# Optimization experiments

Measured on AMD Instinct MI355X. Metric: run time of the kernel, lower is better.

The kernel has to match this reference:

```python
import jax, jax.numpy as jnp
import numpy as np

S, P, D, KH, KW = 1, 1, 1, 3, 3  # stride, padding, dilation, kernel
EPS = 1e-5


def _conv(x, w, b):
    y = jax.lax.conv_general_dilated(
        x, w, (S, S), [(P, P), (P, P)], rhs_dilation=(D, D),
        dimension_numbers=('NCHW', 'OIHW', 'NCHW'))
    return y + b[None, :, None, None]


def _deform_conv(x, offset, mask, w, b):
    # torchvision deform_conv2d v2 semantics: offset layout [B, 2*K, Ho, Wo]
    # with (dy, dx) interleaved per kernel tap; bilinear sampling w/ zero pad.
    B, C, H, W = x.shape
    K = KH * KW
    Ho, Wo = offset.shape[2], offset.shape[3]
    ki, kj = jnp.meshgrid(jnp.arange(KH), jnp.arange(KW), indexing='ij')
    ki = ki.reshape(K).astype(offset.dtype)
    kj = kj.reshape(K).astype(offset.dtype)
    base_y = (jnp.arange(Ho, dtype=offset.dtype) * S - P)[None, None, :, None] + (ki * D)[None, :, None, None]
    base_x = (jnp.arange(Wo, dtype=offset.dtype) * S - P)[None, None, None, :] + (kj * D)[None, :, None, None]
    off = offset.reshape(B, K, 2, Ho, Wo)
    py = base_y + off[:, :, 0]  # [B,K,Ho,Wo]
    px = base_x + off[:, :, 1]
    y0 = jnp.floor(py)
    x0 = jnp.floor(px)
    ly = py - y0
    lx = px - x0
    y0i = y0.astype(jnp.int32)
    x0i = x0.astype(jnp.int32)

    def corner(iy, ix, wgt):
        valid = (iy >= 0) & (iy < H) & (ix >= 0) & (ix < W)
        iyc = jnp.clip(iy, 0, H - 1)
        ixc = jnp.clip(ix, 0, W - 1)
        # gather -> [B, C, K, Ho, Wo]
        v = jax.vmap(lambda img, a, bb: img[:, a, bb])(x, iyc, ixc)
        return v * (wgt * valid)[:, None]

    val = (corner(y0i, x0i, (1 - ly) * (1 - lx))
           + corner(y0i, x0i + 1, (1 - ly) * lx)
           + corner(y0i + 1, x0i, ly * (1 - lx))
           + corner(y0i + 1, x0i + 1, ly * lx))
    val = val * mask[:, None]  # modulation, mask: [B,K,Ho,Wo]
    O = w.shape[0]
    out = jnp.einsum('bckhw,ock->bohw', val, w.reshape(O, C, K))
    return out + b[None, :, None, None]


def setup_inputs() -> dict:
    key = jax.random.key(0)
    ks = jax.random.split(key, 8)
    B, Cin, H, W = 16, 64, 64, 64
    Cout, K = 128, KH * KW
    fan = Cin * K
    x = jax.random.normal(ks[0], (B, Cin, H, W), jnp.float32)
    w_p = jax.random.normal(ks[1], (2 * K, Cin, KH, KW), jnp.float32) * 0.02
    b_p = jax.random.normal(ks[2], (2 * K,), jnp.float32) * 0.01
    w_m = jax.random.normal(ks[3], (K, Cin, KH, KW), jnp.float32) * 0.02
    b_m = jax.random.normal(ks[4], (K,), jnp.float32) * 0.01
    w_d = jax.random.normal(ks[5], (Cout, Cin, KH, KW), jnp.float32) / np.sqrt(fan)
    b_d = jax.random.normal(ks[6], (Cout,), jnp.float32) * 0.01
    gamma = jnp.ones((Cout,), jnp.float32)
    beta = jnp.zeros((Cout,), jnp.float32)
    return {"x": x, "w_p": w_p, "b_p": b_p, "w_m": w_m, "b_m": b_m,
            "w_d": w_d, "b_d": b_d, "gamma": gamma, "beta": beta}


def reference(x, w_p, b_p, w_m, b_m, w_d, b_d, gamma, beta):
    offset = _conv(x, w_p, b_p)                 # [B, 2K, Ho, Wo]
    mask = jax.nn.sigmoid(_conv(x, w_m, b_m))   # [B, K, Ho, Wo]
    y = _deform_conv(x, offset, mask, w_d, b_d)
    # BatchNorm2d (training-mode batch stats, biased variance, eps=1e-5)
    mu = y.mean(axis=(0, 2, 3), keepdims=True)
    var = y.var(axis=(0, 2, 3), keepdims=True)
    yn = (y - mu) * jax.lax.rsqrt(var + EPS)
    yn = yn * gamma[None, :, None, None] + beta[None, :, None, None]
    return jax.nn.gelu(yn, approximate=False)  # nn.GELU default = exact erf
```

## Files before the change

kernel.cpp:

```cpp
#include <hip/hip_runtime.h>
#include <math.h>

#define BB 16
#define CIN 64
#define HH 64
#define WW 64
#define COUT 128
#define HW 4096
#define CK 576
#define VROW 612

typedef __attribute__((ext_vector_type(8))) short short8;
typedef __attribute__((ext_vector_type(4))) short short4v;
typedef __attribute__((ext_vector_type(4))) float f32x4;

#define WT_OFF    0
#define WPM_OFF   36864
#define XH_OFF    46080
#define YB_OFF    2143232
#define SAB_OFF   6337536
#define STAT_OFF  6337792

__device__ __forceinline__ short f2bf(float f) {
    union { float f; unsigned u; } cv; cv.f = f;
    unsigned u = cv.u;
    unsigned r = (u + 0x7fffu + ((u >> 16) & 1u)) >> 16;
    return (short)r;
}
__device__ __forceinline__ float bf2f(short s) {
    union { unsigned u; float f; } cv;
    cv.u = ((unsigned)(unsigned short)s) << 16;
    return cv.f;
}
__device__ __forceinline__ unsigned cvt_pk_bf16(float lo, float hi) {
    unsigned r;
    asm("v_cvt_pk_bf16_f32 %0, %1, %2" : "=v"(r) : "v"(lo), "v"(hi));
    return r;
}

__global__ __launch_bounds__(256) void k_prep(const float* __restrict__ x,
                                              const float* __restrict__ wd,
                                              const float* __restrict__ wp,
                                              const float* __restrict__ wm,
                                              short* __restrict__ xh,
                                              short* __restrict__ wt2,
                                              short* __restrict__ wpm2) {
    const int blk = blockIdx.x;
    if (blk < 1024) {
        __shared__ float t[64][65];
        const int b    = blk >> 6;
        const int pos0 = (blk & 63) << 6;
        const int a    = threadIdx.x & 63;
        const int q    = threadIdx.x >> 6;
#pragma unroll
        for (int i = 0; i < 16; ++i) {
            int c = i * 4 + q;
            t[c][a] = x[((size_t)(b * CIN + c)) * HW + pos0 + a];
        }
        __syncthreads();
#pragma unroll
        for (int i = 0; i < 16; ++i) {
            int p = i * 4 + q;
            xh[((size_t)b * HW + pos0 + p) * CIN + a] = f2bf(t[a][p]);
        }
        return;
    }
    int i = (blk - 1024) * 256 + threadIdx.x;
    if (i < 18 * 128 * 32) {
        int kc  = i >> 12;
        int rem = i & 4095;
        int co  = rem >> 5;
        int kl  = rem & 31;
        int kk  = kc * 32 + kl;
        int k   = kk >> 6;
        int c   = kk & 63;
        wt2[i] = f2bf(wd[co * CK + c * 9 + k]);
        return;
    }
    i -= 18 * 128 * 32;
    if (i < 18 * 32 * 32) {
        int kc  = i >> 10;
        int rem = i & 1023;
        int t   = rem >> 5;
        int kl  = rem & 31;
        int kk  = kc * 32 + kl;
        int k   = kk >> 6;
        int c   = kk & 63;
        float v = 0.f;
        if (t < 18)      v = wp[t * CK + c * 9 + k];
        else if (t < 27) v = wm[(t - 18) * CK + c * 9 + k];
        wpm2[i] = f2bf(v);
    }
}

__device__ __forceinline__ short8 conv_a(const short* __restrict__ xb,
                                         int ho, int wo, int lk, int kc) {
    const int k  = kc >> 1;
    const int c0 = (kc & 1) * 32 + lk * 8;
    const int yy = ho - 1 + k / 3;
    const int xx = wo - 1 + k % 3;
    const bool valid = ((unsigned)yy < 64u) & ((unsigned)xx < 64u);
    const int yyc = min(max(yy, 0), 63);
    const int xxc = min(max(xx, 0), 63);
    short8 a = *(const short8*)&xb[(((yyc << 6) + xxc) << 6) + c0];
    if (!valid) a = (short8)0;
    return a;
}

#define MPB 32
__global__ __launch_bounds__(512) void k_deform(const short* __restrict__ xh,
                                                const short* __restrict__ wt2,
                                                const short* __restrict__ wpm2,
                                                const float* __restrict__ bp,
                                                const float* __restrict__ bm,
                                                const float* __restrict__ bd,
                                                short* __restrict__ yb,
                                                float* __restrict__ gstat) {
    __shared__ short     val[MPB * VROW];
    __shared__ float     s_pm2[2][32][33];
    __shared__ unsigned  s_yx[MPB * 9];
    __shared__ _Float16  s_wh[MPB * 9 * 4];

    const int bid  = blockIdx.x;
    const int swz  = (bid & 7) * 256 + (bid >> 3);
    const int pos0 = swz * MPB;
    const int b   = pos0 >> 12;
    const int ho  = (pos0 >> 6) & 63;
    const int wo0 = pos0 & 63;
    const int tid = threadIdx.x;
    const int wv   = tid >> 6;
    const int lane = tid & 63;
    const int l15  = lane & 15;
    const int lk   = lane >> 4;

    const short* xb = xh + (size_t)b * HW * CIN;

    {
        const int mw = wv & 1;
        const int nw = (wv >> 1) & 1;
        const int kh = wv >> 2;
        const int t  = nw * 16 + l15;
        const short* wr = wpm2 + t * 32 + lk * 8;
        const int wo = wo0 + mw * 16 + l15;
        f32x4 acc = (f32x4)(0.f);
#pragma unroll
        for (int kc = kh * 9; kc < kh * 9 + 9; ++kc) {
            short8 a  = conv_a(xb, ho, wo, lk, kc);
            short8 bf = *(const short8*)&wr[kc * 1024];
            acc = __builtin_amdgcn_mfma_f32_16x16x32_bf16(a, bf, acc, 0, 0, 0);
        }
#pragma unroll
        for (int j = 0; j < 4; ++j)
            s_pm2[kh][t][mw * 16 + lk * 4 + j] = acc[j];
    }
    __syncthreads();

    if (tid < MPB * 9) {
        int k = tid >> 5;
        int p = tid & 31;
        int wo = wo0 + p;
        float dy = s_pm2[0][2 * k    ][p] + s_pm2[1][2 * k    ][p] + bp[2 * k];
        float dx = s_pm2[0][2 * k + 1][p] + s_pm2[1][2 * k + 1][p] + bp[2 * k + 1];
        float mm = s_pm2[0][18 + k   ][p] + s_pm2[1][18 + k   ][p] + bm[k];
        float m  = 1.f / (1.f + expf(-mm));
        float py = (float)(ho - 1 + k / 3) + dy;
        float px = (float)(wo - 1 + k % 3) + dx;
        float fy = floorf(py), fx = floorf(px);
        float ly = py - fy, lx = px - fx;
        int y0 = (int)fy, x0 = (int)fx;
        int y1 = y0 + 1, x1 = x0 + 1;
        float vy0 = ((unsigned)y0 < 64u) ? 1.f : 0.f;
        float vy1 = ((unsigned)y1 < 64u) ? 1.f : 0.f;
        float vx0 = ((unsigned)x0 < 64u) ? 1.f : 0.f;
        float vx1 = ((unsigned)x1 < 64u) ? 1.f : 0.f;
        int y0c = min(max(y0, 0), 63), y1c = min(max(y1, 0), 63);
        int x0c = min(max(x0, 0), 63), x1c = min(max(x1, 0), 63);
        int tt = p * 9 + k;
        s_yx[tt] = (unsigned)y0c | ((unsigned)y1c << 8) | ((unsigned)x0c << 16) | ((unsigned)x1c << 24);
        s_wh[tt * 4 + 0] = (_Float16)((1.f - ly) * (1.f - lx) * m * vy0 * vx0);
        s_wh[tt * 4 + 1] = (_Float16)((1.f - ly) * lx * m * vy0 * vx1);
        s_wh[tt * 4 + 2] = (_Float16)(ly * (1.f - lx) * m * vy1 * vx0);
        s_wh[tt * 4 + 3] = (_Float16)(ly * lx * m * vy1 * vx1);
    }
    __syncthreads();

    {
        const int g  = tid >> 3;
        const int li = tid & 7;
        const int c0 = li * 8;
#pragma unroll
        for (int it = 0; it < 5; ++it) {
            int pr = it * 64 + g;
            if (pr < MPB * 9) {
                unsigned yx = s_yx[pr];
                int y0 = yx & 255, y1 = (yx >> 8) & 255;
                int x0 = (yx >> 16) & 255, x1 = yx >> 24;
                float w0 = (float)s_wh[pr * 4 + 0], w1 = (float)s_wh[pr * 4 + 1];
                float w2 = (float)s_wh[pr * 4 + 2], w3 = (float)s_wh[pr * 4 + 3];
                short8 v00 = *(const short8*)&xb[(((y0 << 6) + x0) << 6) + c0];
                short8 v01 = *(const short8*)&xb[(((y0 << 6) + x1) << 6) + c0];
                short8 v10 = *(const short8*)&xb[(((y1 << 6) + x0) << 6) + c0];
                short8 v11 = *(const short8*)&xb[(((y1 << 6) + x1) << 6) + c0];
                int p = pr / 9, k = pr - p * 9;
                union { unsigned u[4]; short8 s; } pk;
#pragma unroll
                for (int h = 0; h < 4; ++h) {
                    float fa = w0 * bf2f(v00[2*h])   + w1 * bf2f(v01[2*h])
                             + w2 * bf2f(v10[2*h])   + w3 * bf2f(v11[2*h]);
                    float fb = w0 * bf2f(v00[2*h+1]) + w1 * bf2f(v01[2*h+1])
                             + w2 * bf2f(v10[2*h+1]) + w3 * bf2f(v11[2*h+1]);
                    pk.u[h] = cvt_pk_bf16(fa, fb);
                }
                *(short8*)&val[p * VROW + k * 68 + c0] = pk.s;
            }
        }
    }
    __syncthreads();

    f32x4 acc0 = (f32x4)(0.f);
    f32x4 acc1 = (f32x4)(0.f);
    const short* wq = wt2 + (size_t)(wv * 16 + l15) * 32 + lk * 8;
    const int arow0 = l15 * VROW + lk * 8;
    const int arow1 = (l15 + 16) * VROW + lk * 8;
#pragma unroll
    for (int kc = 0; kc < 18; ++kc) {
        const int koff = (kc >> 1) * 68 + (kc & 1) * 32;
        short8 a0 = *(const short8*)&val[arow0 + koff];
        short8 a1 = *(const short8*)&val[arow1 + koff];
        short8 bf = *(const short8*)&wq[kc * 4096];
        acc0 = __builtin_amdgcn_mfma_f32_16x16x32_bf16(a0, bf, acc0, 0, 0, 0);
        acc1 = __builtin_amdgcn_mfma_f32_16x16x32_bf16(a1, bf, acc1, 0, 0, 0);
    }

    const int co = wv * 16 + l15;
    {
        float bias = bd[co];
        short* ybp = yb + ((size_t)(b * COUT + co)) * HW + ho * WW + wo0;
        union { unsigned u[2]; short4v s; } o0, o1;
        o0.u[0] = cvt_pk_bf16(acc0[0] + bias, acc0[1] + bias);
        o0.u[1] = cvt_pk_bf16(acc0[2] + bias, acc0[3] + bias);
        *(short4v*)&ybp[lk * 4] = o0.s;
        o1.u[0] = cvt_pk_bf16(acc1[0] + bias, acc1[1] + bias);
        o1.u[1] = cvt_pk_bf16(acc1[2] + bias, acc1[3] + bias);
        *(short4v*)&ybp[16 + lk * 4] = o1.s;
    }
    float s0 = acc0[0] + acc0[1] + acc0[2] + acc0[3]
             + acc1[0] + acc1[1] + acc1[2] + acc1[3];
    float q0 = acc0[0]*acc0[0] + acc0[1]*acc0[1] + acc0[2]*acc0[2] + acc0[3]*acc0[3]
             + acc1[0]*acc1[0] + acc1[1]*acc1[1] + acc1[2]*acc1[2] + acc1[3]*acc1[3];
    s0 += __shfl_xor(s0, 16); s0 += __shfl_xor(s0, 32);
    q0 += __shfl_xor(q0, 16); q0 += __shfl_xor(q0, 32);
    if (lane < 16) {
        float* slot = gstat + (bid & 63) * 256;
        atomicAdd(&slot[wv * 16 + lane],       s0);
        atomicAdd(&slot[128 + wv * 16 + lane], q0);
    }
}

__global__ __launch_bounds__(128) void k_finalize(const float* __restrict__ gstat,
                                                  const float* __restrict__ bd,
                                                  const float* __restrict__ gamma,
                                                  const float* __restrict__ beta,
                                                  float* __restrict__ sAB) {
    int c = threadIdx.x;
    float s = 0.f, q = 0.f;
    for (int sl = 0; sl < 64; ++sl) {
        s += gstat[sl * 256 + c];
        q += gstat[sl * 256 + 128 + c];
    }
    const float invN = 1.f / (float)(BB * HW);
    float mean_acc = s * invN;
    float var = q * invN - mean_acc * mean_acc;
    float mean_y = mean_acc + bd[c];
    float A = gamma[c] * rsqrtf(var + 1e-5f);
    sAB[c]       = A;
    sAB[128 + c] = beta[c] - mean_y * A;
}

__global__ __launch_bounds__(256) void k_norm_gelu(const short* __restrict__ yb,
                                                   const float* __restrict__ sAB,
                                                   float* __restrict__ out) {
    int i8 = blockIdx.x * 256 + threadIdx.x;
    if (i8 >= (BB * COUT * HW) / 8) return;
    int c = (i8 >> 9) & 127;
    float A  = sAB[c];
    float Bc = sAB[128 + c];
    short8 v = *(const short8*)&yb[(size_t)i8 * 8];
    float4 r0, r1;
    float t;
    t = bf2f(v[0]) * A + Bc; r0.x = 0.5f * t * (1.f + erff(t * 0.70710678118654752f));
    t = bf2f(v[1]) * A + Bc; r0.y = 0.5f * t * (1.f + erff(t * 0.70710678118654752f));
    t = bf2f(v[2]) * A + Bc; r0.z = 0.5f * t * (1.f + erff(t * 0.70710678118654752f));
    t = bf2f(v[3]) * A + Bc; r0.w = 0.5f * t * (1.f + erff(t * 0.70710678118654752f));
    t = bf2f(v[4]) * A + Bc; r1.x = 0.5f * t * (1.f + erff(t * 0.70710678118654752f));
    t = bf2f(v[5]) * A + Bc; r1.y = 0.5f * t * (1.f + erff(t * 0.70710678118654752f));
    t = bf2f(v[6]) * A + Bc; r1.z = 0.5f * t * (1.f + erff(t * 0.70710678118654752f));
    t = bf2f(v[7]) * A + Bc; r1.w = 0.5f * t * (1.f + erff(t * 0.70710678118654752f));
    *(float4*)&out[(size_t)i8 * 8]     = r0;
    *(float4*)&out[(size_t)i8 * 8 + 4] = r1;
}

extern "C" void kernel_launch(void* const* d_in, const int* in_sizes, int n_in,
                              void* d_out, int out_size, void* d_ws, size_t ws_size,
                              hipStream_t stream) {
    const float* x     = (const float*)d_in[0];
    const float* w_p   = (const float*)d_in[1];
    const float* b_p   = (const float*)d_in[2];
    const float* w_m   = (const float*)d_in[3];
    const float* b_m   = (const float*)d_in[4];
    const float* w_d   = (const float*)d_in[5];
    const float* b_d   = (const float*)d_in[6];
    const float* gamma = (const float*)d_in[7];
    const float* beta  = (const float*)d_in[8];
    float* ws  = (float*)d_ws;
    float* out = (float*)d_out;

    short* wt2  = (short*)(ws + WT_OFF);
    short* wpm2 = (short*)(ws + WPM_OFF);
    short* xh   = (short*)(ws + XH_OFF);
    short* yb   = (short*)(ws + YB_OFF);
    float* sAB  = ws + SAB_OFF;
    float* gstat= ws + STAT_OFF;

    hipMemsetAsync(gstat, 0, 64 * 256 * sizeof(float), stream);
    k_prep<<<dim3(1024 + 360), dim3(256), 0, stream>>>(x, w_d, w_p, w_m, xh, wt2, wpm2);
    k_deform<<<dim3(BB * HW / MPB), dim3(512), 0, stream>>>(xh, wt2, wpm2, b_p, b_m, b_d, yb, gstat);
    k_finalize<<<dim3(1), dim3(128), 0, stream>>>(gstat, b_d, gamma, beta, sAB);
    k_norm_gelu<<<dim3(BB * COUT * HW / 8 / 256), dim3(256), 0, stream>>>(yb, sAB, out);
}
```

Measured before the change: 86.45 us.

## Software-pipeline global loads in deform kernel phases with inline asm waitcnt

Replaces the compiler-scheduled loops in the offset conv, the bilinear gather and the main MFMA loop with manually multi-buffered global loads issued through inline asm. Explicit s_waitcnt vmcnt values keep several loads in flight while earlier MFMAs or blends execute. The finalize reduction is split into four independent accumulators. This is meant to hide global memory latency, at the cost of more registers and fragile hand-counted waitcnt values that the compiler cannot check.

After: 84.50 us. -2.3%, faster.

```diff
diff --git a/kernel.cpp b/kernel.cpp
--- a/kernel.cpp
+++ b/kernel.cpp
@@ -93,20 +93,6 @@
     }
 }
 
-__device__ __forceinline__ short8 conv_a(const short* __restrict__ xb,
-                                         int ho, int wo, int lk, int kc) {
-    const int k  = kc >> 1;
-    const int c0 = (kc & 1) * 32 + lk * 8;
-    const int yy = ho - 1 + k / 3;
-    const int xx = wo - 1 + k % 3;
-    const bool valid = ((unsigned)yy < 64u) & ((unsigned)xx < 64u);
-    const int yyc = min(max(yy, 0), 63);
-    const int xxc = min(max(xx, 0), 63);
-    short8 a = *(const short8*)&xb[(((yyc << 6) + xxc) << 6) + c0];
-    if (!valid) a = (short8)0;
-    return a;
-}
-
 #define MPB 32
 __global__ __launch_bounds__(512) void k_deform(const short* __restrict__ xh,
                                                 const short* __restrict__ wt2,
@@ -136,19 +122,49 @@
     const short* xb = xh + (size_t)b * HW * CIN;
 
     {
-        const int mw = wv & 1;
-        const int nw = (wv >> 1) & 1;
-        const int kh = wv >> 2;
-        const int t  = nw * 16 + l15;
+        const int mw  = wv & 1;
+        const int nw  = (wv >> 1) & 1;
+        const int kh  = wv >> 2;
+        const int kc0 = kh * 9;
+        const int t   = nw * 16 + l15;
         const short* wr = wpm2 + t * 32 + lk * 8;
         const int wo = wo0 + mw * 16 + l15;
+
+        short8 ab[3], bb[3];
+        int    va[3];
+
+#define P0_ISSUE(slot, kcl)                                                  \
+        {   int kc = kc0 + (kcl);                                            \
+            int k = kc >> 1; int c0 = (kc & 1) * 32 + lk * 8;                \
+            int yy = ho - 1 + k / 3;                                         \
+            int xx = wo - 1 + k % 3;                                         \
+            va[slot] = (((unsigned)yy < 64u) & ((unsigned)xx < 64u)) ? -1 : 0; \
+            int yyc = min(max(yy, 0), 63), xxc = min(max(xx, 0), 63);        \
+            const short* ap_ = xb + (((yyc << 6) + xxc) << 6) + c0;          \
+            const short* bp_ = wr + kc * 1024;                               \
+            asm volatile("global_load_dwordx4 %0, %1, off"                   \
+                         : "=&v"(ab[slot]) : "v"(ap_));                      \
+            asm volatile("global_load_dwordx4 %0, %1, off"                   \
+                         : "=&v"(bb[slot]) : "v"(bp_));                      \
+        }
+
+#define P0_STEP(i, VM)                                                      \
+        {   asm volatile("s_waitcnt vmcnt(" #VM ")"                          \
+                         : "+v"(ab[(i) % 3]), "+v"(bb[(i) % 3]));            \
+            short8 a = ab[(i) % 3];                                          \
+            if (!va[(i) % 3]) a = (short8)0;                                 \
+            acc = __builtin_amdgcn_mfma_f32_16x16x32_bf16(a, bb[(i) % 3], acc, 0, 0, 0); \
+            if ((i) + 3 < 9) P0_ISSUE((i) % 3, (i) + 3);                     \
+        }
+
         f32x4 acc = (f32x4)(0.f);
-#pragma unroll
-        for (int kc = kh * 9; kc < kh * 9 + 9; ++kc) {
-            short8 a  = conv_a(xb, ho, wo, lk, kc);
-            short8 bf = *(const short8*)&wr[kc * 1024];
-            acc = __builtin_amdgcn_mfma_f32_16x16x32_bf16(a, bf, acc, 0, 0, 0);
-        }
+        P0_ISSUE(0, 0) P0_ISSUE(1, 1) P0_ISSUE(2, 2)
+        P0_STEP(0, 4) P0_STEP(1, 4) P0_STEP(2, 4)
+        P0_STEP(3, 4) P0_STEP(4, 4) P0_STEP(5, 4)
+        P0_STEP(6, 4) P0_STEP(7, 2) P0_STEP(8, 0)
+#undef P0_ISSUE
+#undef P0_STEP
+
 #pragma unroll
         for (int j = 0; j < 4; ++j)
             s_pm2[kh][t][mw * 16 + lk * 4 + j] = acc[j];
@@ -188,31 +204,73 @@
         const int g  = tid >> 3;
         const int li = tid & 7;
         const int c0 = li * 8;
-#pragma unroll
-        for (int it = 0; it < 5; ++it) {
-            int pr = it * 64 + g;
-            if (pr < MPB * 9) {
-                unsigned yx = s_yx[pr];
-                int y0 = yx & 255, y1 = (yx >> 8) & 255;
-                int x0 = (yx >> 16) & 255, x1 = yx >> 24;
-                float w0 = (float)s_wh[pr * 4 + 0], w1 = (float)s_wh[pr * 4 + 1];
-                float w2 = (float)s_wh[pr * 4 + 2], w3 = (float)s_wh[pr * 4 + 3];
-                short8 v00 = *(const short8*)&xb[(((y0 << 6) + x0) << 6) + c0];
-                short8 v01 = *(const short8*)&xb[(((y0 << 6) + x1) << 6) + c0];
-                short8 v10 = *(const short8*)&xb[(((y1 << 6) + x0) << 6) + c0];
-                short8 v11 = *(const short8*)&xb[(((y1 << 6) + x1) << 6) + c0];
-                int p = pr / 9, k = pr - p * 9;
-                union { unsigned u[4]; short8 s; } pk;
-#pragma unroll
-                for (int h = 0; h < 4; ++h) {
-                    float fa = w0 * bf2f(v00[2*h])   + w1 * bf2f(v01[2*h])
-                             + w2 * bf2f(v10[2*h])   + w3 * bf2f(v11[2*h]);
-                    float fb = w0 * bf2f(v00[2*h+1]) + w1 * bf2f(v01[2*h+1])
-                             + w2 * bf2f(v10[2*h+1]) + w3 * bf2f(v11[2*h+1]);
-                    pk.u[h] = cvt_pk_bf16(fa, fb);
-                }
-                *(short8*)&val[p * VROW + k * 68 + c0] = pk.s;
+        short8 cb[2][4];
+
+#define P2_ISSUE(slot, IT)                                                   \
+        {   int pr = (IT) * 64 + g;                                          \
+            unsigned yx = s_yx[pr];                                          \
+            int y0 = yx & 255, y1 = (yx >> 8) & 255;                         \
+            int x0 = (yx >> 16) & 255, x1 = yx >> 24;                        \
+            asm volatile("global_load_dwordx4 %0, %1, off"                   \
+                : "=&v"(cb[slot][0]) : "v"(xb + (((y0 << 6) + x0) << 6) + c0)); \
+            asm volatile("global_load_dwordx4 %0, %1, off"                   \
+                : "=&v"(cb[slot][1]) : "v"(xb + (((y0 << 6) + x1) << 6) + c0)); \
+            asm volatile("global_load_dwordx4 %0, %1, off"                   \
+                : "=&v"(cb[slot][2]) : "v"(xb + (((y1 << 6) + x0) << 6) + c0)); \
+            asm volatile("global_load_dwordx4 %0, %1, off"                   \
+                : "=&v"(cb[slot][3]) : "v"(xb + (((y1 << 6) + x1) << 6) + c0)); \
+        }
+
+#define P2_BLEND(slot, IT, VM)                                               \
+        {   asm volatile("s_waitcnt vmcnt(" #VM ")"                          \
+                : "+v"(cb[slot][0]), "+v"(cb[slot][1]),                      \
+                  "+v"(cb[slot][2]), "+v"(cb[slot][3]));                     \
+            int pr = (IT) * 64 + g;                                          \
+            int p = pr / 9, k = pr - p * 9;                                  \
+            float w0 = (float)s_wh[pr * 4 + 0], w1 = (float)s_wh[pr * 4 + 1];\
+            float w2 = (float)s_wh[pr * 4 + 2], w3 = (float)s_wh[pr * 4 + 3];\
+            union { unsigned u[4]; short8 s; } pk;                           \
+            _Pragma("unroll")                                                \
+            for (int h = 0; h < 4; ++h) {                                    \
+                float fa = w0*bf2f(cb[slot][0][2*h])   + w1*bf2f(cb[slot][1][2*h])   \
+                         + w2*bf2f(cb[slot][2][2*h])   + w3*bf2f(cb[slot][3][2*h]);  \
+                float fb = w0*bf2f(cb[slot][0][2*h+1]) + w1*bf2f(cb[slot][1][2*h+1]) \
+                         + w2*bf2f(cb[slot][2][2*h+1]) + w3*bf2f(cb[slot][3][2*h+1]);\
+                pk.u[h] = cvt_pk_bf16(fa, fb);                               \
+            }                                                                \
+            *(short8*)&val[p * VROW + k * 68 + c0] = pk.s;                   \
+        }
+
+        P2_ISSUE(0, 0)
+        P2_ISSUE(1, 1) P2_BLEND(0, 0, 4)
+        P2_ISSUE(0, 2) P2_BLEND(1, 1, 4)
+        P2_ISSUE(1, 3) P2_BLEND(0, 2, 4)
+        P2_BLEND(1, 3, 0)
+#undef P2_ISSUE
+#undef P2_BLEND
+
+        if (g < 32) {
+            int pr = 256 + g;
+            unsigned yx = s_yx[pr];
+            int y0 = yx & 255, y1 = (yx >> 8) & 255;
+            int x0 = (yx >> 16) & 255, x1 = yx >> 24;
+            float w0 = (float)s_wh[pr * 4 + 0], w1 = (float)s_wh[pr * 4 + 1];
+            float w2 = (float)s_wh[pr * 4 + 2], w3 = (float)s_wh[pr * 4 + 3];
+            short8 v00 = *(const short8*)&xb[(((y0 << 6) + x0) << 6) + c0];
+            short8 v01 = *(const short8*)&xb[(((y0 << 6) + x1) << 6) + c0];
+            short8 v10 = *(const short8*)&xb[(((y1 << 6) + x0) << 6) + c0];
+            short8 v11 = *(const short8*)&xb[(((y1 << 6) + x1) << 6) + c0];
+            int p = pr / 9, k = pr - p * 9;
+            union { unsigned u[4]; short8 s; } pk;
+#pragma unroll
+            for (int h = 0; h < 4; ++h) {
+                float fa = w0 * bf2f(v00[2*h])   + w1 * bf2f(v01[2*h])
+                         + w2 * bf2f(v10[2*h])   + w3 * bf2f(v11[2*h]);
+                float fb = w0 * bf2f(v00[2*h+1]) + w1 * bf2f(v01[2*h+1])
+                         + w2 * bf2f(v10[2*h+1]) + w3 * bf2f(v11[2*h+1]);
+                pk.u[h] = cvt_pk_bf16(fa, fb);
             }
+            *(short8*)&val[p * VROW + k * 68 + c0] = pk.s;
         }
     }
     __syncthreads();
@@ -222,14 +280,31 @@
     const short* wq = wt2 + (size_t)(wv * 16 + l15) * 32 + lk * 8;
     const int arow0 = l15 * VROW + lk * 8;
     const int arow1 = (l15 + 16) * VROW + lk * 8;
-#pragma unroll
-    for (int kc = 0; kc < 18; ++kc) {
-        const int koff = (kc >> 1) * 68 + (kc & 1) * 32;
-        short8 a0 = *(const short8*)&val[arow0 + koff];
-        short8 a1 = *(const short8*)&val[arow1 + koff];
-        short8 bf = *(const short8*)&wq[kc * 4096];
-        acc0 = __builtin_amdgcn_mfma_f32_16x16x32_bf16(a0, bf, acc0, 0, 0, 0);
-        acc1 = __builtin_amdgcn_mfma_f32_16x16x32_bf16(a1, bf, acc1, 0, 0, 0);
+    {
+        short8 bbf[4];
+
+#define P3_ISSUE(slot, kc)                                                   \
+        asm volatile("global_load_dwordx4 %0, %1, off"                       \
+                     : "=&v"(bbf[slot]) : "v"(wq + (kc) * 4096));
+
+#define P3_STEP(i, VM)                                                       \
+        {   const int koff = ((i) >> 1) * 68 + ((i) & 1) * 32;               \
+            short8 a0 = *(const short8*)&val[arow0 + koff];                  \
+            short8 a1 = *(const short8*)&val[arow1 + koff];                  \
+            asm volatile("s_waitcnt vmcnt(" #VM ")" : "+v"(bbf[(i) & 3]));   \
+            acc0 = __builtin_amdgcn_mfma_f32_16x16x32_bf16(a0, bbf[(i) & 3], acc0, 0, 0, 0); \
+            acc1 = __builtin_amdgcn_mfma_f32_16x16x32_bf16(a1, bbf[(i) & 3], acc1, 0, 0, 0); \
+            if ((i) + 4 < 18) P3_ISSUE((i) & 3, (i) + 4);                    \
+        }
+
+        P3_ISSUE(0, 0) P3_ISSUE(1, 1) P3_ISSUE(2, 2) P3_ISSUE(3, 3)
+        P3_STEP(0, 3)  P3_STEP(1, 3)  P3_STEP(2, 3)  P3_STEP(3, 3)
+        P3_STEP(4, 3)  P3_STEP(5, 3)  P3_STEP(6, 3)  P3_STEP(7, 3)
+        P3_STEP(8, 3)  P3_STEP(9, 3)  P3_STEP(10, 3) P3_STEP(11, 3)
+        P3_STEP(12, 3) P3_STEP(13, 3) P3_STEP(14, 3) P3_STEP(15, 2)
+        P3_STEP(16, 1) P3_STEP(17, 0)
+#undef P3_ISSUE
+#undef P3_STEP
     }
 
     const int co = wv * 16 + l15;
@@ -263,11 +338,18 @@
                                                   const float* __restrict__ beta,
                                                   float* __restrict__ sAB) {
     int c = threadIdx.x;
-    float s = 0.f, q = 0.f;
-    for (int sl = 0; sl < 64; ++sl) {
-        s += gstat[sl * 256 + c];
-        q += gstat[sl * 256 + 128 + c];
-    }
+    float sa[4] = {0.f, 0.f, 0.f, 0.f};
+    float qa[4] = {0.f, 0.f, 0.f, 0.f};
+#pragma unroll
+    for (int sl = 0; sl < 64; sl += 4) {
+#pragma unroll
+        for (int j = 0; j < 4; ++j) {
+            sa[j] += gstat[(sl + j) * 256 + c];
+            qa[j] += gstat[(sl + j) * 256 + 128 + c];
+        }
+    }
+    float s = (sa[0] + sa[1]) + (sa[2] + sa[3]);
+    float q = (qa[0] + qa[1]) + (qa[2] + qa[3]);
     const float invN = 1.f / (float)(BB * HW);
     float mean_acc = s * invN;
     float var = q * invN - mean_acc * mean_acc;
```

## Switch intermediates from bf16 to fp16 with packed half2 bilinear sampling

Applied to the files above, without the earlier changes.

Converts the staged input, weights, sampled-value tile and pre-norm output from bf16 to fp16, uses the fp16 MFMA, and replaces the per-element fp32 bilinear interpolation with packed __hfma2 operations on broadcast half2 weights. The aim is to cut ALU work in the gather/interpolation stage. It also vectorizes the x transpose loads in the prep kernel, trims the unused rows of the offset/mask conv result buffer, and splits the finalize reduction into four accumulators. The cost is fp16 range and precision risk: the interpolation now accumulates in half precision, and the pre-norm activations are stored in fp16.

Result: faster. 83.78 us (median of 2 runs) (-3.1%).

```diff
diff --git a/kernel.cpp b/kernel.cpp
--- a/kernel.cpp
+++ b/kernel.cpp
@@ -1,4 +1,5 @@
 #include <hip/hip_runtime.h>
+#include <hip/hip_fp16.h>
 #include <math.h>
 
 #define BB 16
@@ -10,6 +11,8 @@
 #define CK 576
 #define VROW 612
 
+typedef _Float16 f16;
+typedef __attribute__((ext_vector_type(8))) _Float16 f16x8;
 typedef __attribute__((ext_vector_type(8))) short short8;
 typedef __attribute__((ext_vector_type(4))) short short4v;
 typedef __attribute__((ext_vector_type(4))) float f32x4;
@@ -21,47 +24,47 @@
 #define SAB_OFF   6337536
 #define STAT_OFF  6337792
 
-__device__ __forceinline__ short f2bf(float f) {
-    union { float f; unsigned u; } cv; cv.f = f;
-    unsigned u = cv.u;
-    unsigned r = (u + 0x7fffu + ((u >> 16) & 1u)) >> 16;
-    return (short)r;
-}
-__device__ __forceinline__ float bf2f(short s) {
-    union { unsigned u; float f; } cv;
-    cv.u = ((unsigned)(unsigned short)s) << 16;
-    return cv.f;
-}
-__device__ __forceinline__ unsigned cvt_pk_bf16(float lo, float hi) {
-    unsigned r;
-    asm("v_cvt_pk_bf16_f32 %0, %1, %2" : "=v"(r) : "v"(lo), "v"(hi));
-    return r;
-}
+union U8h { short8 s; __half2 h[4]; f16x8 f; };
+union U4h { short4v s; __half2 h[2]; };
+union UWh { unsigned u; __half2 h; };
 
 __global__ __launch_bounds__(256) void k_prep(const float* __restrict__ x,
                                               const float* __restrict__ wd,
                                               const float* __restrict__ wp,
                                               const float* __restrict__ wm,
-                                              short* __restrict__ xh,
-                                              short* __restrict__ wt2,
-                                              short* __restrict__ wpm2) {
+                                              f16* __restrict__ xh,
+                                              f16* __restrict__ wt2,
+                                              f16* __restrict__ wpm2) {
     const int blk = blockIdx.x;
     if (blk < 1024) {
         __shared__ float t[64][65];
         const int b    = blk >> 6;
         const int pos0 = (blk & 63) << 6;
-        const int a    = threadIdx.x & 63;
-        const int q    = threadIdx.x >> 6;
-#pragma unroll
-        for (int i = 0; i < 16; ++i) {
-            int c = i * 4 + q;
-            t[c][a] = x[((size_t)(b * CIN + c)) * HW + pos0 + a];
+        {
+            const int c4 = threadIdx.x & 15;
+            const int cc = threadIdx.x >> 4;
+#pragma unroll
+            for (int j = 0; j < 4; ++j) {
+                int c = cc + j * 16;
+                float4 v = *(const float4*)&x[((size_t)(b * CIN + c)) * HW + pos0 + c4 * 4];
+                t[c][c4 * 4 + 0] = v.x;
+                t[c][c4 * 4 + 1] = v.y;
+                t[c][c4 * 4 + 2] = v.z;
+                t[c][c4 * 4 + 3] = v.w;
+            }
         }
         __syncthreads();
-#pragma unroll
-        for (int i = 0; i < 16; ++i) {
-            int p = i * 4 + q;
-            xh[((size_t)b * HW + pos0 + p) * CIN + a] = f2bf(t[a][p]);
+        {
+            const int a2 = (threadIdx.x & 31) * 2;
+            const int q  = threadIdx.x >> 5;
+#pragma unroll
+            for (int i = 0; i < 8; ++i) {
+                int p = i * 8 + q;
+                __half2 hv = __halves2half2(__float2half(t[a2][p]),
+                                            __float2half(t[a2 + 1][p]));
+                UWh u; u.h = hv;
+                *(unsigned*)&xh[((size_t)b * HW + pos0 + p) * CIN + a2] = u.u;
+            }
         }
         return;
     }
@@ -74,7 +77,7 @@
         int kk  = kc * 32 + kl;
         int k   = kk >> 6;
         int c   = kk & 63;
-        wt2[i] = f2bf(wd[co * CK + c * 9 + k]);
+        wt2[i] = (f16)wd[co * CK + c * 9 + k];
         return;
     }
     i -= 18 * 128 * 32;
@@ -89,12 +92,12 @@
         float v = 0.f;
         if (t < 18)      v = wp[t * CK + c * 9 + k];
         else if (t < 27) v = wm[(t - 18) * CK + c * 9 + k];
-        wpm2[i] = f2bf(v);
-    }
-}
-
-__device__ __forceinline__ short8 conv_a(const short* __restrict__ xb,
-                                         int ho, int wo, int lk, int kc) {
+        wpm2[i] = (f16)v;
+    }
+}
+
+__device__ __forceinline__ f16x8 conv_a(const f16* __restrict__ xb,
+                                        int ho, int wo, int lk, int kc) {
     const int k  = kc >> 1;
     const int c0 = (kc & 1) * 32 + lk * 8;
     const int yy = ho - 1 + k / 3;
@@ -102,24 +105,24 @@
     const bool valid = ((unsigned)yy < 64u) & ((unsigned)xx < 64u);
     const int yyc = min(max(yy, 0), 63);
     const int xxc = min(max(xx, 0), 63);
-    short8 a = *(const short8*)&xb[(((yyc << 6) + xxc) << 6) + c0];
-    if (!valid) a = (short8)0;
+    f16x8 a = *(const f16x8*)&xb[(((yyc << 6) + xxc) << 6) + c0];
+    if (!valid) a = (f16x8)0;
     return a;
 }
 
 #define MPB 32
-__global__ __launch_bounds__(512) void k_deform(const short* __restrict__ xh,
-                                                const short* __restrict__ wt2,
-                                                const short* __restrict__ wpm2,
+__global__ __launch_bounds__(512) void k_deform(const f16* __restrict__ xh,
+                                                const f16* __restrict__ wt2,
+                                                const f16* __restrict__ wpm2,
                                                 const float* __restrict__ bp,
                                                 const float* __restrict__ bm,
                                                 const float* __restrict__ bd,
-                                                short* __restrict__ yb,
+                                                f16* __restrict__ yb,
                                                 float* __restrict__ gstat) {
-    __shared__ short     val[MPB * VROW];
-    __shared__ float     s_pm2[2][32][33];
+    __shared__ f16       val[MPB * VROW];
+    __shared__ float     s_pm2[2][28][33];
     __shared__ unsigned  s_yx[MPB * 9];
-    __shared__ _Float16  s_wh[MPB * 9 * 4];
+    __shared__ unsigned  s_w[MPB * 9 * 4];
 
     const int bid  = blockIdx.x;
     const int swz  = (bid & 7) * 256 + (bid >> 3);
@@ -133,25 +136,27 @@
     const int l15  = lane & 15;
     const int lk   = lane >> 4;
 
-    const short* xb = xh + (size_t)b * HW * CIN;
+    const f16* xb = xh + (size_t)b * HW * CIN;
 
     {
         const int mw = wv & 1;
         const int nw = (wv >> 1) & 1;
         const int kh = wv >> 2;
         const int t  = nw * 16 + l15;
-        const short* wr = wpm2 + t * 32 + lk * 8;
+        const f16* wr = wpm2 + t * 32 + lk * 8;
         const int wo = wo0 + mw * 16 + l15;
         f32x4 acc = (f32x4)(0.f);
 #pragma unroll
         for (int kc = kh * 9; kc < kh * 9 + 9; ++kc) {
-            short8 a  = conv_a(xb, ho, wo, lk, kc);
-            short8 bf = *(const short8*)&wr[kc * 1024];
-            acc = __builtin_amdgcn_mfma_f32_16x16x32_bf16(a, bf, acc, 0, 0, 0);
-        }
-#pragma unroll
-        for (int j = 0; j < 4; ++j)
-            s_pm2[kh][t][mw * 16 + lk * 4 + j] = acc[j];
+            f16x8 a  = conv_a(xb, ho, wo, lk, kc);
+            f16x8 bf = *(const f16x8*)&wr[kc * 1024];
+            acc = __builtin_amdgcn_mfma_f32_16x16x32_f16(a, bf, acc, 0, 0, 0);
+        }
+        if (t < 28) {
+#pragma unroll
+            for (int j = 0; j < 4; ++j)
+                s_pm2[kh][t][mw * 16 + lk * 4 + j] = acc[j];
+        }
     }
     __syncthreads();
 
@@ -177,10 +182,14 @@
         int x0c = min(max(x0, 0), 63), x1c = min(max(x1, 0), 63);
         int tt = p * 9 + k;
         s_yx[tt] = (unsigned)y0c | ((unsigned)y1c << 8) | ((unsigned)x0c << 16) | ((unsigned)x1c << 24);
-        s_wh[tt * 4 + 0] = (_Float16)((1.f - ly) * (1.f - lx) * m * vy0 * vx0);
-        s_wh[tt * 4 + 1] = (_Float16)((1.f - ly) * lx * m * vy0 * vx1);
-        s_wh[tt * 4 + 2] = (_Float16)(ly * (1.f - lx) * m * vy1 * vx0);
-        s_wh[tt * 4 + 3] = (_Float16)(ly * lx * m * vy1 * vx1);
+        float w0 = (1.f - ly) * (1.f - lx) * m * vy0 * vx0;
+        float w1 = (1.f - ly) * lx * m * vy0 * vx1;
+        float w2 = ly * (1.f - lx) * m * vy1 * vx0;
+        float w3 = ly * lx * m * vy1 * vx1;
+        s_w[tt * 4 + 0] = (unsigned)__half_as_ushort(__float2half(w0)) * 0x10001u;
+        s_w[tt * 4 + 1] = (unsigned)__half_as_ushort(__float2half(w1)) * 0x10001u;
+        s_w[tt * 4 + 2] = (unsigned)__half_as_ushort(__float2half(w2)) * 0x10001u;
+        s_w[tt * 4 + 3] = (unsigned)__half_as_ushort(__float2half(w3)) * 0x10001u;
     }
     __syncthreads();
 
@@ -195,23 +204,25 @@
                 unsigned yx = s_yx[pr];
                 int y0 = yx & 255, y1 = (yx >> 8) & 255;
                 int x0 = (yx >> 16) & 255, x1 = yx >> 24;
-                float w0 = (float)s_wh[pr * 4 + 0], w1 = (float)s_wh[pr * 4 + 1];
-                float w2 = (float)s_wh[pr * 4 + 2], w3 = (float)s_wh[pr * 4 + 3];
-                short8 v00 = *(const short8*)&xb[(((y0 << 6) + x0) << 6) + c0];
-                short8 v01 = *(const short8*)&xb[(((y0 << 6) + x1) << 6) + c0];
-                short8 v10 = *(const short8*)&xb[(((y1 << 6) + x0) << 6) + c0];
-                short8 v11 = *(const short8*)&xb[(((y1 << 6) + x1) << 6) + c0];
+                UWh w0u, w1u, w2u, w3u;
+                w0u.u = s_w[pr * 4 + 0];
+                w1u.u = s_w[pr * 4 + 1];
+                w2u.u = s_w[pr * 4 + 2];
+                w3u.u = s_w[pr * 4 + 3];
+                U8h v00, v01, v10, v11, o;
+                v00.s = *(const short8*)&xb[(((y0 << 6) + x0) << 6) + c0];
+                v01.s = *(const short8*)&xb[(((y0 << 6) + x1) << 6) + c0];
+                v10.s = *(const short8*)&xb[(((y1 << 6) + x0) << 6) + c0];
+                v11.s = *(const short8*)&xb[(((y1 << 6) + x1) << 6) + c0];
                 int p = pr / 9, k = pr - p * 9;
-                union { unsigned u[4]; short8 s; } pk;
-#pragma unroll
-                for (int h = 0; h < 4; ++h) {
-                    float fa = w0 * bf2f(v00[2*h])   + w1 * bf2f(v01[2*h])
-                             + w2 * bf2f(v10[2*h])   + w3 * bf2f(v11[2*h]);
-                    float fb = w0 * bf2f(v00[2*h+1]) + w1 * bf2f(v01[2*h+1])
-                             + w2 * bf2f(v10[2*h+1]) + w3 * bf2f(v11[2*h+1]);
-                    pk.u[h] = cvt_pk_bf16(fa, fb);
+#pragma unroll
+                for (int h2 = 0; h2 < 4; ++h2) {
+                    o.h[h2] = __hfma2(v00.h[h2], w0u.h,
+                              __hfma2(v01.h[h2], w1u.h,
+                              __hfma2(v10.h[h2], w2u.h,
+                              __hmul2(v11.h[h2], w3u.h))));
                 }
-                *(short8*)&val[p * VROW + k * 68 + c0] = pk.s;
+                *(short8*)&val[p * VROW + k * 68 + c0] = o.s;
             }
         }
     }
@@ -219,29 +230,29 @@
 
     f32x4 acc0 = (f32x4)(0.f);
     f32x4 acc1 = (f32x4)(0.f);
-    const short* wq = wt2 + (size_t)(wv * 16 + l15) * 32 + lk * 8;
+    const f16* wq = wt2 + (size_t)(wv * 16 + l15) * 32 + lk * 8;
     const int arow0 = l15 * VROW + lk * 8;
     const int arow1 = (l15 + 16) * VROW + lk * 8;
 #pragma unroll
     for (int kc = 0; kc < 18; ++kc) {
         const int koff = (kc >> 1) * 68 + (kc & 1) * 32;
-        short8 a0 = *(const short8*)&val[arow0 + koff];
-        short8 a1 = *(const short8*)&val[arow1 + koff];
-        short8 bf = *(const short8*)&wq[kc * 4096];
-        acc0 = __builtin_amdgcn_mfma_f32_16x16x32_bf16(a0, bf, acc0, 0, 0, 0);
-        acc1 = __builtin_amdgcn_mfma_f32_16x16x32_bf16(a1, bf, acc1, 0, 0, 0);
+        f16x8 a0 = *(const f16x8*)&val[arow0 + koff];
+        f16x8 a1 = *(const f16x8*)&val[arow1 + koff];
+        f16x8 bf = *(const f16x8*)&wq[kc * 4096];
+        acc0 = __builtin_amdgcn_mfma_f32_16x16x32_f16(a0, bf, acc0, 0, 0, 0);
+        acc1 = __builtin_amdgcn_mfma_f32_16x16x32_f16(a1, bf, acc1, 0, 0, 0);
     }
 
     const int co = wv * 16 + l15;
     {
         float bias = bd[co];
-        short* ybp = yb + ((size_t)(b * COUT + co)) * HW + ho * WW + wo0;
-        union { unsigned u[2]; short4v s; } o0, o1;
-        o0.u[0] = cvt_pk_bf16(acc0[0] + bias, acc0[1] + bias);
-        o0.u[1] = cvt_pk_bf16(acc0[2] + bias, acc0[3] + bias);
+        f16* ybp = yb + ((size_t)(b * COUT + co)) * HW + ho * WW + wo0;
+        U4h o0, o1;
+        o0.h[0] = __halves2half2(__float2half(acc0[0] + bias), __float2half(acc0[1] + bias));
+        o0.h[1] = __halves2half2(__float2half(acc0[2] + bias), __float2half(acc0[3] + bias));
         *(short4v*)&ybp[lk * 4] = o0.s;
-        o1.u[0] = cvt_pk_bf16(acc1[0] + bias, acc1[1] + bias);
-        o1.u[1] = cvt_pk_bf16(acc1[2] + bias, acc1[3] + bias);
+        o1.h[0] = __halves2half2(__float2half(acc1[0] + bias), __float2half(acc1[1] + bias));
+        o1.h[1] = __halves2half2(__float2half(acc1[2] + bias), __float2half(acc1[3] + bias));
         *(short4v*)&ybp[16 + lk * 4] = o1.s;
     }
     float s0 = acc0[0] + acc0[1] + acc0[2] + acc0[3]
@@ -263,11 +274,18 @@
                                                   const float* __restrict__ beta,
                                                   float* __restrict__ sAB) {
     int c = threadIdx.x;
-    float s = 0.f, q = 0.f;
-    for (int sl = 0; sl < 64; ++sl) {
-        s += gstat[sl * 256 + c];
-        q += gstat[sl * 256 + 128 + c];
-    }
+    float sa[4] = {0.f, 0.f, 0.f, 0.f};
+    float qa[4] = {0.f, 0.f, 0.f, 0.f};
+#pragma unroll
+    for (int sl = 0; sl < 64; sl += 4) {
+#pragma unroll
+        for (int j = 0; j < 4; ++j) {
+            sa[j] += gstat[(sl + j) * 256 + c];
+            qa[j] += gstat[(sl + j) * 256 + 128 + c];
+        }
+    }
+    float s = (sa[0] + sa[1]) + (sa[2] + sa[3]);
+    float q = (qa[0] + qa[1]) + (qa[2] + qa[3]);
     const float invN = 1.f / (float)(BB * HW);
     float mean_acc = s * invN;
     float var = q * invN - mean_acc * mean_acc;
@@ -277,7 +295,7 @@
     sAB[128 + c] = beta[c] - mean_y * A;
 }
 
-__global__ __launch_bounds__(256) void k_norm_gelu(const short* __restrict__ yb,
+__global__ __launch_bounds__(256) void k_norm_gelu(const f16* __restrict__ yb,
                                                    const float* __restrict__ sAB,
                                                    float* __restrict__ out) {
     int i8 = blockIdx.x * 256 + threadIdx.x;
@@ -285,17 +303,17 @@
     int c = (i8 >> 9) & 127;
     float A  = sAB[c];
     float Bc = sAB[128 + c];
-    short8 v = *(const short8*)&yb[(size_t)i8 * 8];
+    f16x8 v = *(const f16x8*)&yb[(size_t)i8 * 8];
     float4 r0, r1;
     float t;
-    t = bf2f(v[0]) * A + Bc; r0.x = 0.5f * t * (1.f + erff(t * 0.70710678118654752f));
-    t = bf2f(v[1]) * A + Bc; r0.y = 0.5f * t * (1.f + erff(t * 0.70710678118654752f));
-    t = bf2f(v[2]) * A + Bc; r0.z = 0.5f * t * (1.f + erff(t * 0.70710678118654752f));
-    t = bf2f(v[3]) * A + Bc; r0.w = 0.5f * t * (1.f + erff(t * 0.70710678118654752f));
-    t = bf2f(v[4]) * A + Bc; r1.x = 0.5f * t * (1.f + erff(t * 0.70710678118654752f));
-    t = bf2f(v[5]) * A + Bc; r1.y = 0.5f * t * (1.f + erff(t * 0.70710678118654752f));
-    t = bf2f(v[6]) * A + Bc; r1.z = 0.5f * t * (1.f + erff(t * 0.70710678118654752f));
-    t = bf2f(v[7]) * A + Bc; r1.w = 0.5f * t * (1.f + erff(t * 0.70710678118654752f));
+    t = (float)v[0] * A + Bc; r0.x = 0.5f * t * (1.f + erff(t * 0.70710678118654752f));
+    t = (float)v[1] * A + Bc; r0.y = 0.5f * t * (1.f + erff(t * 0.70710678118654752f));
+    t = (float)v[2] * A + Bc; r0.z = 0.5f * t * (1.f + erff(t * 0.70710678118654752f));
+    t = (float)v[3] * A + Bc; r0.w = 0.5f * t * (1.f + erff(t * 0.70710678118654752f));
+    t = (float)v[4] * A + Bc; r1.x = 0.5f * t * (1.f + erff(t * 0.70710678118654752f));
+    t = (float)v[5] * A + Bc; r1.y = 0.5f * t * (1.f + erff(t * 0.70710678118654752f));
+    t = (float)v[6] * A + Bc; r1.z = 0.5f * t * (1.f + erff(t * 0.70710678118654752f));
+    t = (float)v[7] * A + Bc; r1.w = 0.5f * t * (1.f + erff(t * 0.70710678118654752f));
     *(float4*)&out[(size_t)i8 * 8]     = r0;
     *(float4*)&out[(size_t)i8 * 8 + 4] = r1;
 }
@@ -315,10 +333,10 @@
     float* ws  = (float*)d_ws;
     float* out = (float*)d_out;
 
-    short* wt2  = (short*)(ws + WT_OFF);
-    short* wpm2 = (short*)(ws + WPM_OFF);
-    short* xh   = (short*)(ws + XH_OFF);
-    short* yb   = (short*)(ws + YB_OFF);
+    f16*  wt2  = (f16*)(ws + WT_OFF);
+    f16*  wpm2 = (f16*)(ws + WPM_OFF);
+    f16*  xh   = (f16*)(ws + XH_OFF);
+    f16*  yb   = (f16*)(ws + YB_OFF);
     float* sAB  = ws + SAB_OFF;
     float* gstat= ws + STAT_OFF;
 
```
